# Optimization experiments

Measured on AMD Instinct MI355X. Metric: run time of the kernel, lower is better.

Reference implementation:

```python
import jax, jax.numpy as jnp
import numpy as np
import math

N_HEADS = 8

def setup_inputs() -> dict:
    key = jax.random.key(0)
    qkv = jax.random.normal(key, (4, 1536, 2048), dtype=jnp.float32)
    return {"qkv": qkv}

def reference(qkv) -> jnp.ndarray:
    bs, width, length = qkv.shape
    assert width % (3 * N_HEADS) == 0
    ch = width // (3 * N_HEADS)
    q, k, v = jnp.split(qkv, 3, axis=1)  # each [bs, n_heads*ch, length]
    scale = 1.0 / math.sqrt(math.sqrt(ch))
    q = (q * scale).reshape(bs * N_HEADS, ch, length)
    k = (k * scale).reshape(bs * N_HEADS, ch, length)
    v = v.reshape(bs * N_HEADS, ch, length)
    # scores: [B*H, t, s]
    weight = jnp.einsum('bct,bcs->bts', q, k)
    weight = jax.nn.softmax(weight, axis=-1)
    a = jnp.einsum('bts,bcs->bct', weight, v)  # [B*H, ch, length]
    return a.reshape(bs, -1, length)
```

## Files before the change

### kernel.cpp

```cpp
#include <hip/hip_runtime.h>
#include <hip/hip_bf16.h>

typedef unsigned short u16;
typedef unsigned int u32;
typedef __attribute__((ext_vector_type(8))) short short8;
typedef __attribute__((ext_vector_type(16))) float f32x16;

#define SEQ 2048

__device__ __forceinline__ u16 f2bf(float f) {
  union { __hip_bfloat16 h; u16 u; } c;
  c.h = __float2bfloat16(f);
  return c.u;
}

__device__ __forceinline__ float exp2fast(float x) {
  return __builtin_amdgcn_exp2f(x);
}

__global__ __launch_bounds__(256) void prep_qk(const float* __restrict__ qkv,
                                               u16* __restrict__ wsQ,
                                               u16* __restrict__ wsK) {
  __shared__ float tile[64 * 67];
  const int tid = threadIdx.x;
  const int t0 = blockIdx.x * 64;
  const int bh = blockIdx.y;
  const int b = bh >> 3, h = bh & 7;
  const int isK = blockIdx.z;
  const float scale = 0.42466090014692505f;
  const size_t inbase = ((size_t)b * 1536 + (size_t)isK * 512 + (size_t)h * 64) * SEQ;

  const int c = tid >> 2, tq = tid & 3;
#pragma unroll
  for (int u = 0; u < 4; ++u) {
    const int t = tq * 16 + u * 4;
    const float4 v = *(const float4*)(qkv + inbase + (size_t)c * SEQ + t0 + t);
    tile[c * 67 + t + 0] = v.x * scale;
    tile[c * 67 + t + 1] = v.y * scale;
    tile[c * 67 + t + 2] = v.z * scale;
    tile[c * 67 + t + 3] = v.w * scale;
  }
  __syncthreads();
  const int tt = tid >> 2, cq = tid & 3, c0 = cq * 16;
  u16* dst = (isK ? wsK : wsQ) + ((size_t)bh * SEQ + t0 + tt) * 64 + c0;
  union { u16 us[8]; uint4 v; } p0, p1;
#pragma unroll
  for (int i = 0; i < 8; ++i) p0.us[i] = f2bf(tile[(c0 + i) * 67 + tt]);
#pragma unroll
  for (int i = 0; i < 8; ++i) p1.us[i] = f2bf(tile[(c0 + 8 + i) * 67 + tt]);
  *(uint4*)(dst) = p0.v;
  *(uint4*)(dst + 8) = p1.v;
}

__global__ __launch_bounds__(256) void prep_v(const float* __restrict__ qkv,
                                              u16* __restrict__ wsV) {
  const int idx = blockIdx.x * 256 + threadIdx.x;
  const int s4 = idx & 511;
  const int cc = (idx >> 9) & 63;
  const int bh = idx >> 15;
  const int b = bh >> 3, h = bh & 7;
  const float4 v = *(const float4*)(qkv + (((size_t)b * 1536 + 1024 + (size_t)h * 64 + cc) * SEQ) + (size_t)s4 * 4);
  union { u16 us[4]; uint2 d; } pk;
  pk.us[0] = f2bf(v.x); pk.us[1] = f2bf(v.y); pk.us[2] = f2bf(v.z); pk.us[3] = f2bf(v.w);
  *(uint2*)(wsV + ((size_t)bh * 64 + cc) * SEQ + (size_t)s4 * 4) = pk.d;
}

__global__ __launch_bounds__(512, 2) void attn_kernel(const u16* __restrict__ wsQ,
                                                      const u16* __restrict__ wsK,
                                                      const u16* __restrict__ wsV,
                                                      float* __restrict__ out) {
  __shared__ __align__(16) char smem[65536];
  __shared__ float Xl[4][2][32];

  const int tid = threadIdx.x;
  const int w = tid >> 6;
  const int lane = tid & 63;
  const int tl = lane & 31;
  const int hi = lane >> 5;
  const int sh = w >> 2;
  const int u = w & 3;
  const int ts = tid & 255;

  const int bid = blockIdx.x;
  const int vb = (bid & 7) * 32 + (bid >> 3);
  const int tblk = vb & 7, bh = vb >> 3;
  const int tq0 = tblk * 256 + u * 64;

  const u16* qb = wsQ + (size_t)bh * (SEQ * 64);
  const u16* kb = wsK + (size_t)bh * (SEQ * 64);
  const u16* vbp = wsV + (size_t)bh * (SEQ * 64);

  char* KVs = smem + sh * 32768;

  short8 qf[2][4];
#pragma unroll
  for (int cb = 0; cb < 2; ++cb) {
    const u16* qrow = qb + (size_t)(tq0 + cb * 32 + tl) * 64 + 8 * hi;
#pragma unroll
    for (int ks = 0; ks < 4; ++ks) qf[cb][ks] = *(const short8*)(qrow + 16 * ks);
  }

  f32x16 acc[4];
#pragma unroll
  for (int a = 0; a < 4; ++a)
#pragma unroll
    for (int r = 0; r < 16; ++r) acc[a][r] = 0.0f;
  float la0[4] = {0, 0, 0, 0};
  float la1[4] = {0, 0, 0, 0};

  const int s_base = sh * 1024;
  const int srow = ts >> 3;
  uint4 kg[2], vg[2];

#define STAGE_LOAD(S)                                                       \
  do {                                                                      \
    _Pragma("unroll")                                                       \
    for (int _it = 0; _it < 2; ++_it) {                                     \
      const int _idx = _it * 256 + ts;                                      \
      const int _row = _idx >> 3, _g = _idx & 7;                            \
      kg[_it] = *(const uint4*)(kb + (size_t)((S) + _row) * 64 + _g * 8);   \
      vg[_it] = *(const uint4*)(vbp + (size_t)_row * SEQ + (S) + _g * 8);   \
    }                                                                       \
  } while (0)

#define STAGE_WRITE(PBUF)                                                   \
  do {                                                                      \
    char* _kd = KVs + (PBUF) * 16384;                                       \
    _Pragma("unroll")                                                       \
    for (int _it = 0; _it < 2; ++_it) {                                     \
      const int _idx = _it * 256 + ts;                                      \
      const int _row = _idx >> 3, _g = _idx & 7;                            \
      const int _sw = (_g ^ (_row & 7)) << 4;                               \
      *(uint4*)(_kd + _row * 128 + _sw) = kg[_it];                          \
      *(uint4*)(_kd + 8192 + _row * 128 + _sw) = vg[_it];                   \
    }                                                                       \
  } while (0)

#define PACK_P(PV16, PF0, PF1)                                                        \
  do {                                                                                \
    u32 _pk[8];                                                                       \
    _Pragma("unroll")                                                                 \
    for (int _q = 0; _q < 8; ++_q) {                                                  \
      const float _lo = PV16[2 * _q], _hi = PV16[2 * _q + 1];                         \
      asm("v_cvt_pk_bf16_f32 %0, %1, %2" : "=v"(_pk[_q]) : "v"(_lo), "v"(_hi));       \
    }                                                                                 \
    asm("v_permlane32_swap_b32 %0, %1" : "+v"(_pk[0]), "+v"(_pk[2]));                 \
    asm("v_permlane32_swap_b32 %0, %1" : "+v"(_pk[1]), "+v"(_pk[3]));                 \
    asm("v_permlane32_swap_b32 %0, %1" : "+v"(_pk[4]), "+v"(_pk[6]));                 \
    asm("v_permlane32_swap_b32 %0, %1" : "+v"(_pk[5]), "+v"(_pk[7]));                 \
    union { u32 u[4]; short8 v; } _f0, _f1;                                           \
    _f0.u[0] = _pk[0]; _f0.u[1] = _pk[1]; _f0.u[2] = _pk[2]; _f0.u[3] = _pk[3];       \
    _f1.u[0] = _pk[4]; _f1.u[1] = _pk[5]; _f1.u[2] = _pk[6]; _f1.u[3] = _pk[7];       \
    PF0 = _f0.v; PF1 = _f1.v;                                                         \
  } while (0)

  STAGE_LOAD(s_base);
  STAGE_WRITE(0);
  __syncthreads();

  int p = 0;
  for (int i = 0; i < 16; ++i) {
    if (i < 15) {
      const int snext = s_base + ((i + 1) << 6);
      STAGE_LOAD(snext);
    }

    const char* Ks = KVs + p * 16384;
    const char* Vs = Ks + 8192;

#pragma unroll
    for (int ss = 0; ss < 2; ++ss) {
      const int krow = ss * 32 + tl;
      short8 kf[4];
#pragma unroll
      for (int ks = 0; ks < 4; ++ks)
        kf[ks] = *(const short8*)(Ks + krow * 128 + (((2 * ks + hi) ^ (krow & 7)) << 4));

      f32x16 s0 = {0, 0, 0, 0, 0, 0, 0, 0, 0, 0, 0, 0, 0, 0, 0, 0};
      f32x16 s1 = s0;
      __builtin_amdgcn_s_setprio(1);
#pragma unroll
      for (int ks = 0; ks < 4; ++ks) {
        s0 = __builtin_amdgcn_mfma_f32_32x32x16_bf16(kf[ks], qf[0][ks], s0, 0, 0, 0);
        s1 = __builtin_amdgcn_mfma_f32_32x32x16_bf16(kf[ks], qf[1][ks], s1, 0, 0, 0);
      }
      __builtin_amdgcn_s_setprio(0);

#pragma unroll
      for (int r = 0; r < 16; ++r) s0[r] = exp2fast(s0[r]);
#pragma unroll
      for (int r = 0; r < 16; ++r) s1[r] = exp2fast(s1[r]);
#pragma unroll
      for (int j = 0; j < 4; ++j) {
        la0[j] += (s0[4 * j] + s0[4 * j + 1]) + (s0[4 * j + 2] + s0[4 * j + 3]);
        la1[j] += (s1[4 * j] + s1[4 * j + 1]) + (s1[4 * j + 2] + s1[4 * j + 3]);
      }

      short8 pf00, pf01, pf10, pf11;
      PACK_P(s0, pf00, pf01);
      PACK_P(s1, pf10, pf11);

      __builtin_amdgcn_s_setprio(1);
#pragma unroll
      for (int ct = 0; ct < 2; ++ct) {
        const int vrow = ct * 32 + tl;
#pragma unroll
        for (int ks2 = 0; ks2 < 2; ++ks2) {
          const int gr = ss * 4 + 2 * ks2 + hi;
          const short8 vf = *(const short8*)(Vs + vrow * 128 + ((gr ^ (vrow & 7)) << 4));
          acc[0 + ct] = __builtin_amdgcn_mfma_f32_32x32x16_bf16(vf, ks2 ? pf01 : pf00, acc[0 + ct], 0, 0, 0);
          acc[2 + ct] = __builtin_amdgcn_mfma_f32_32x32x16_bf16(vf, ks2 ? pf11 : pf10, acc[2 + ct], 0, 0, 0);
        }
      }
      __builtin_amdgcn_s_setprio(0);
    }

    if (i < 15) STAGE_WRITE(p ^ 1);
    __syncthreads();
    p ^= 1;
  }

  float l0 = (la0[0] + la0[1]) + (la0[2] + la0[3]);
  float l1 = (la1[0] + la1[1]) + (la1[2] + la1[3]);
  l0 += __shfl_xor(l0, 32, 64);
  l1 += __shfl_xor(l1, 32, 64);

  float* Xa = (float*)smem + u * 4096;
  if (sh == 1) {
#pragma unroll
    for (int a = 0; a < 4; ++a)
#pragma unroll
      for (int r = 0; r < 16; ++r) Xa[(a * 16 + r) * 64 + lane] = acc[a][r];
    Xl[u][0][tl] = l0;
    Xl[u][1][tl] = l1;
  }
  __syncthreads();
  if (sh == 0) {
    float* ob = out + (size_t)bh * 64 * SEQ;
    const float inv0 = 1.0f / (l0 + Xl[u][0][tl]);
    const float inv1 = 1.0f / (l1 + Xl[u][1][tl]);
#pragma unroll
    for (int ct = 0; ct < 2; ++ct)
#pragma unroll
      for (int r = 0; r < 16; ++r) {
        const int c = ct * 32 + (r & 3) + 8 * (r >> 2) + 4 * hi;
        const int ta = tq0 + tl, tb2 = tq0 + 32 + tl;
        ob[(size_t)c * SEQ + ta] = (acc[0 + ct][r] + Xa[((0 + ct) * 16 + r) * 64 + lane]) * inv0;
        ob[(size_t)c * SEQ + tb2] = (acc[2 + ct][r] + Xa[((2 + ct) * 16 + r) * 64 + lane]) * inv1;
      }
  }
}

extern "C" void kernel_launch(void* const* d_in, const int* in_sizes, int n_in,
                              void* d_out, int out_size, void* d_ws, size_t ws_size,
                              hipStream_t stream) {
  const float* qkv = (const float*)d_in[0];
  float* out = (float*)d_out;
  u16* wsQ = (u16*)d_ws;
  u16* wsK = wsQ + (size_t)32 * SEQ * 64;
  u16* wsV = wsK + (size_t)32 * SEQ * 64;

  prep_qk<<<dim3(32, 32, 2), 256, 0, stream>>>(qkv, wsQ, wsK);
  prep_v<<<4096, 256, 0, stream>>>(qkv, wsV);
  attn_kernel<<<256, 512, 0, stream>>>(wsQ, wsK, wsV, out);
}
```

Baseline: 60.65 us.

## Pre-swizzle K/V into LDS-ready chunks and stage with global_load_lds

The prep kernels now write K and V into a combined workspace laid out in 32KB chunks that already match the swizzled shared-memory layout. The attention kernel copies each chunk straight into LDS with global_load_lds, removing the register round-trip of the old load-then-write staging. The grid grows to 512 blocks of 128 queries each, with four waves splitting the keys per unit and a two-step cross-wave reduction at the end. The launch bounds ask for four blocks per CU, which may raise occupancy but adds register pressure, more reduction work, and more blocks re-reading K/V.

```diff
diff --git a/kernel.cpp b/kernel.cpp
--- a/kernel.cpp
+++ b/kernel.cpp
@@ -18,9 +18,10 @@
   return __builtin_amdgcn_exp2f(x);
 }
 
+
 __global__ __launch_bounds__(256) void prep_qk(const float* __restrict__ qkv,
                                                u16* __restrict__ wsQ,
-                                               u16* __restrict__ wsK) {
+                                               u16* __restrict__ wsKV) {
   __shared__ float tile[64 * 67];
   const int tid = threadIdx.x;
   const int t0 = blockIdx.x * 64;
@@ -41,56 +42,74 @@
     tile[c * 67 + t + 3] = v.w * scale;
   }
   __syncthreads();
-  const int tt = tid >> 2, cq = tid & 3, c0 = cq * 16;
-  u16* dst = (isK ? wsK : wsQ) + ((size_t)bh * SEQ + t0 + tt) * 64 + c0;
-  union { u16 us[8]; uint4 v; } p0, p1;
-#pragma unroll
-  for (int i = 0; i < 8; ++i) p0.us[i] = f2bf(tile[(c0 + i) * 67 + tt]);
-#pragma unroll
-  for (int i = 0; i < 8; ++i) p1.us[i] = f2bf(tile[(c0 + 8 + i) * 67 + tt]);
-  *(uint4*)(dst) = p0.v;
-  *(uint4*)(dst + 8) = p1.v;
+
+  if (isK) {
+    const int tt = tid >> 2, cq = tid & 3;
+    const int j = (t0 >> 5) + (tt >> 5);
+    const int row = tt & 31;
+    u16* base = wsKV + (size_t)bh * 262144
+              + (size_t)(j >> 2) * 16384 + (size_t)((j >> 1) & 1) * 8192
+              + (size_t)(j & 1) * 2048 + row * 64;
+    union { u16 us[8]; uint4 q; } g0, g1;
+#pragma unroll
+    for (int e = 0; e < 8; ++e) g0.us[e] = f2bf(tile[(cq * 16 + e) * 67 + tt]);
+#pragma unroll
+    for (int e = 0; e < 8; ++e) g1.us[e] = f2bf(tile[(cq * 16 + 8 + e) * 67 + tt]);
+    *(uint4*)(base + (((2 * cq) ^ (row & 7)) << 3)) = g0.q;
+    *(uint4*)(base + (((2 * cq + 1) ^ (row & 7)) << 3)) = g1.q;
+  } else {
+    const int tt = tid >> 2, cq = tid & 3, c0 = cq * 16;
+    u16* dst = wsQ + ((size_t)bh * SEQ + t0 + tt) * 64 + c0;
+    union { u16 us[8]; uint4 v; } p0, p1;
+#pragma unroll
+    for (int i = 0; i < 8; ++i) p0.us[i] = f2bf(tile[(c0 + i) * 67 + tt]);
+#pragma unroll
+    for (int i = 0; i < 8; ++i) p1.us[i] = f2bf(tile[(c0 + 8 + i) * 67 + tt]);
+    *(uint4*)(dst) = p0.v;
+    *(uint4*)(dst + 8) = p1.v;
+  }
 }
 
 __global__ __launch_bounds__(256) void prep_v(const float* __restrict__ qkv,
-                                              u16* __restrict__ wsV) {
+                                              u16* __restrict__ wsKV) {
   const int idx = blockIdx.x * 256 + threadIdx.x;
-  const int s4 = idx & 511;
-  const int cc = (idx >> 9) & 63;
-  const int bh = idx >> 15;
+  const int sg = idx & 7;
+  const int g64 = (idx >> 3) & 31;
+  const int cc = (idx >> 8) & 63;
+  const int bh = idx >> 14;
   const int b = bh >> 3, h = bh & 7;
-  const float4 v = *(const float4*)(qkv + (((size_t)b * 1536 + 1024 + (size_t)h * 64 + cc) * SEQ) + (size_t)s4 * 4);
-  union { u16 us[4]; uint2 d; } pk;
-  pk.us[0] = f2bf(v.x); pk.us[1] = f2bf(v.y); pk.us[2] = f2bf(v.z); pk.us[3] = f2bf(v.w);
-  *(uint2*)(wsV + ((size_t)bh * 64 + cc) * SEQ + (size_t)s4 * 4) = pk.d;
-}
-
-__global__ __launch_bounds__(512, 2) void attn_kernel(const u16* __restrict__ wsQ,
-                                                      const u16* __restrict__ wsK,
-                                                      const u16* __restrict__ wsV,
+  const float* src = qkv + ((size_t)b * 1536 + 1024 + (size_t)h * 64 + cc) * SEQ + g64 * 64 + sg * 8;
+  const float4 v0 = *(const float4*)(src);
+  const float4 v1 = *(const float4*)(src + 4);
+  union { u16 us[8]; uint4 q; } pk;
+  pk.us[0] = f2bf(v0.x); pk.us[1] = f2bf(v0.y); pk.us[2] = f2bf(v0.z); pk.us[3] = f2bf(v0.w);
+  pk.us[4] = f2bf(v1.x); pk.us[5] = f2bf(v1.y); pk.us[6] = f2bf(v1.z); pk.us[7] = f2bf(v1.w);
+  u16* dst = wsKV + (size_t)bh * 262144 + (size_t)(g64 >> 1) * 16384 + (size_t)(g64 & 1) * 8192
+           + 4096 + cc * 64 + ((sg ^ (cc & 7)) << 3);
+  *(uint4*)dst = pk.q;
+}
+
+__global__ __launch_bounds__(512, 4) void attn_kernel(const u16* __restrict__ wsQ,
+                                                      const u16* __restrict__ wsKV,
                                                       float* __restrict__ out) {
   __shared__ __align__(16) char smem[65536];
-  __shared__ float Xl[4][2][32];
+  __shared__ float Xl[2][2][2][32];
 
   const int tid = threadIdx.x;
   const int w = tid >> 6;
   const int lane = tid & 63;
   const int tl = lane & 31;
   const int hi = lane >> 5;
-  const int sh = w >> 2;
-  const int u = w & 3;
-  const int ts = tid & 255;
+  const int unit = w >> 2;
+  const int sp = w & 3;
 
   const int bid = blockIdx.x;
-  const int vb = (bid & 7) * 32 + (bid >> 3);
-  const int tblk = vb & 7, bh = vb >> 3;
-  const int tq0 = tblk * 256 + u * 64;
+  const int vb = (bid & 7) * 64 + (bid >> 3);
+  const int tbp = vb & 15, bh = vb >> 4;
+  const int tq0 = tbp * 128 + unit * 64;
 
   const u16* qb = wsQ + (size_t)bh * (SEQ * 64);
-  const u16* kb = wsK + (size_t)bh * (SEQ * 64);
-  const u16* vbp = wsV + (size_t)bh * (SEQ * 64);
-
-  char* KVs = smem + sh * 32768;
+  const char* kvb = (const char*)(wsKV + (size_t)bh * 262144);
 
   short8 qf[2][4];
 #pragma unroll
@@ -108,32 +127,15 @@
   float la0[4] = {0, 0, 0, 0};
   float la1[4] = {0, 0, 0, 0};
 
-  const int s_base = sh * 1024;
-  const int srow = ts >> 3;
-  uint4 kg[2], vg[2];
-
-#define STAGE_LOAD(S)                                                       \
-  do {                                                                      \
-    _Pragma("unroll")                                                       \
-    for (int _it = 0; _it < 2; ++_it) {                                     \
-      const int _idx = _it * 256 + ts;                                      \
-      const int _row = _idx >> 3, _g = _idx & 7;                            \
-      kg[_it] = *(const uint4*)(kb + (size_t)((S) + _row) * 64 + _g * 8);   \
-      vg[_it] = *(const uint4*)(vbp + (size_t)_row * SEQ + (S) + _g * 8);   \
-    }                                                                       \
-  } while (0)
-
-#define STAGE_WRITE(PBUF)                                                   \
-  do {                                                                      \
-    char* _kd = KVs + (PBUF) * 16384;                                       \
-    _Pragma("unroll")                                                       \
-    for (int _it = 0; _it < 2; ++_it) {                                     \
-      const int _idx = _it * 256 + ts;                                      \
-      const int _row = _idx >> 3, _g = _idx & 7;                            \
-      const int _sw = (_g ^ (_row & 7)) << 4;                               \
-      *(uint4*)(_kd + _row * 128 + _sw) = kg[_it];                          \
-      *(uint4*)(_kd + 8192 + _row * 128 + _sw) = vg[_it];                   \
-    }                                                                       \
+#define STAGE(QUAD, BUF)                                                              \
+  do {                                                                                \
+    const char* _s = kvb + (size_t)(QUAD) * 32768 + w * 4096 + lane * 16;             \
+    char* _d = smem + (BUF) * 32768 + w * 4096;                                       \
+    _Pragma("unroll")                                                                 \
+    for (int _c = 0; _c < 4; ++_c)                                                    \
+      __builtin_amdgcn_global_load_lds(                                               \
+          (__attribute__((address_space(1))) void*)(_s + _c * 1024),                  \
+          (__attribute__((address_space(3))) void*)(_d + _c * 1024), 16, 0, 0);       \
   } while (0)
 
 #define PACK_P(PV16, PF0, PF1)                                                        \
@@ -154,70 +156,60 @@
     PF0 = _f0.v; PF1 = _f1.v;                                                         \
   } while (0)
 
-  STAGE_LOAD(s_base);
-  STAGE_WRITE(0);
-  __syncthreads();
-
-  int p = 0;
+  STAGE(0, 0);
+  __syncthreads();
+
   for (int i = 0; i < 16; ++i) {
-    if (i < 15) {
-      const int snext = s_base + ((i + 1) << 6);
-      STAGE_LOAD(snext);
-    }
-
-    const char* Ks = KVs + p * 16384;
-    const char* Vs = Ks + 8192;
-
-#pragma unroll
-    for (int ss = 0; ss < 2; ++ss) {
-      const int krow = ss * 32 + tl;
-      short8 kf[4];
-#pragma unroll
-      for (int ks = 0; ks < 4; ++ks)
-        kf[ks] = *(const short8*)(Ks + krow * 128 + (((2 * ks + hi) ^ (krow & 7)) << 4));
-
-      f32x16 s0 = {0, 0, 0, 0, 0, 0, 0, 0, 0, 0, 0, 0, 0, 0, 0, 0};
-      f32x16 s1 = s0;
-      __builtin_amdgcn_s_setprio(1);
-#pragma unroll
-      for (int ks = 0; ks < 4; ++ks) {
-        s0 = __builtin_amdgcn_mfma_f32_32x32x16_bf16(kf[ks], qf[0][ks], s0, 0, 0, 0);
-        s1 = __builtin_amdgcn_mfma_f32_32x32x16_bf16(kf[ks], qf[1][ks], s1, 0, 0, 0);
+    if (i < 15) STAGE(i + 1, (i + 1) & 1);
+
+    const char* grp = smem + (i & 1) * 32768 + (sp >> 1) * 16384;
+    const char* Ks = grp + (sp & 1) * 4096;
+    const char* Vs = grp + 8192;
+
+    short8 kf[4];
+#pragma unroll
+    for (int ks = 0; ks < 4; ++ks)
+      kf[ks] = *(const short8*)(Ks + tl * 128 + (((2 * ks + hi) ^ (tl & 7)) << 4));
+
+    f32x16 s0 = {0, 0, 0, 0, 0, 0, 0, 0, 0, 0, 0, 0, 0, 0, 0, 0};
+    f32x16 s1 = s0;
+    __builtin_amdgcn_s_setprio(1);
+#pragma unroll
+    for (int ks = 0; ks < 4; ++ks) {
+      s0 = __builtin_amdgcn_mfma_f32_32x32x16_bf16(kf[ks], qf[0][ks], s0, 0, 0, 0);
+      s1 = __builtin_amdgcn_mfma_f32_32x32x16_bf16(kf[ks], qf[1][ks], s1, 0, 0, 0);
+    }
+    __builtin_amdgcn_s_setprio(0);
+
+#pragma unroll
+    for (int r = 0; r < 16; ++r) s0[r] = exp2fast(s0[r]);
+#pragma unroll
+    for (int r = 0; r < 16; ++r) s1[r] = exp2fast(s1[r]);
+#pragma unroll
+    for (int j = 0; j < 4; ++j) {
+      la0[j] += (s0[4 * j] + s0[4 * j + 1]) + (s0[4 * j + 2] + s0[4 * j + 3]);
+      la1[j] += (s1[4 * j] + s1[4 * j + 1]) + (s1[4 * j + 2] + s1[4 * j + 3]);
+    }
+
+    short8 pf00, pf01, pf10, pf11;
+    PACK_P(s0, pf00, pf01);
+    PACK_P(s1, pf10, pf11);
+
+    __builtin_amdgcn_s_setprio(1);
+#pragma unroll
+    for (int ct = 0; ct < 2; ++ct) {
+      const int vrow = ct * 32 + tl;
+#pragma unroll
+      for (int ks2 = 0; ks2 < 2; ++ks2) {
+        const int gr = (sp & 1) * 4 + 2 * ks2 + hi;
+        const short8 vf = *(const short8*)(Vs + vrow * 128 + ((gr ^ (vrow & 7)) << 4));
+        acc[0 + ct] = __builtin_amdgcn_mfma_f32_32x32x16_bf16(vf, ks2 ? pf01 : pf00, acc[0 + ct], 0, 0, 0);
+        acc[2 + ct] = __builtin_amdgcn_mfma_f32_32x32x16_bf16(vf, ks2 ? pf11 : pf10, acc[2 + ct], 0, 0, 0);
       }
-      __builtin_amdgcn_s_setprio(0);
-
-#pragma unroll
-      for (int r = 0; r < 16; ++r) s0[r] = exp2fast(s0[r]);
-#pragma unroll
-      for (int r = 0; r < 16; ++r) s1[r] = exp2fast(s1[r]);
-#pragma unroll
-      for (int j = 0; j < 4; ++j) {
-        la0[j] += (s0[4 * j] + s0[4 * j + 1]) + (s0[4 * j + 2] + s0[4 * j + 3]);
-        la1[j] += (s1[4 * j] + s1[4 * j + 1]) + (s1[4 * j + 2] + s1[4 * j + 3]);
-      }
-
-      short8 pf00, pf01, pf10, pf11;
-      PACK_P(s0, pf00, pf01);
-      PACK_P(s1, pf10, pf11);
-
-      __builtin_amdgcn_s_setprio(1);
-#pragma unroll
-      for (int ct = 0; ct < 2; ++ct) {
-        const int vrow = ct * 32 + tl;
-#pragma unroll
-        for (int ks2 = 0; ks2 < 2; ++ks2) {
-          const int gr = ss * 4 + 2 * ks2 + hi;
-          const short8 vf = *(const short8*)(Vs + vrow * 128 + ((gr ^ (vrow & 7)) << 4));
-          acc[0 + ct] = __builtin_amdgcn_mfma_f32_32x32x16_bf16(vf, ks2 ? pf01 : pf00, acc[0 + ct], 0, 0, 0);
-          acc[2 + ct] = __builtin_amdgcn_mfma_f32_32x32x16_bf16(vf, ks2 ? pf11 : pf10, acc[2 + ct], 0, 0, 0);
-        }
-      }
-      __builtin_amdgcn_s_setprio(0);
-    }
-
-    if (i < 15) STAGE_WRITE(p ^ 1);
+    }
+    __builtin_amdgcn_s_setprio(0);
+
     __syncthreads();
-    p ^= 1;
   }
 
   float l0 = (la0[0] + la0[1]) + (la0[2] + la0[3]);
@@ -225,29 +217,48 @@
   l0 += __shfl_xor(l0, 32, 64);
   l1 += __shfl_xor(l1, 32, 64);
 
-  float* Xa = (float*)smem + u * 4096;
-  if (sh == 1) {
+  if (sp >= 2) {
+    float* Xa = (float*)smem + (size_t)(unit * 2 + (sp - 2)) * 4096;
 #pragma unroll
     for (int a = 0; a < 4; ++a)
 #pragma unroll
       for (int r = 0; r < 16; ++r) Xa[(a * 16 + r) * 64 + lane] = acc[a][r];
-    Xl[u][0][tl] = l0;
-    Xl[u][1][tl] = l1;
-  }
-  __syncthreads();
-  if (sh == 0) {
+    Xl[unit][sp - 2][0][tl] = l0;
+    Xl[unit][sp - 2][1][tl] = l1;
+  }
+  __syncthreads();
+  if (sp < 2) {
+    float* Xa = (float*)smem + (size_t)(unit * 2 + sp) * 4096;
+#pragma unroll
+    for (int a = 0; a < 4; ++a)
+#pragma unroll
+      for (int r = 0; r < 16; ++r) acc[a][r] += Xa[(a * 16 + r) * 64 + lane];
+    l0 += Xl[unit][sp][0][tl];
+    l1 += Xl[unit][sp][1][tl];
+    if (sp == 1) {
+#pragma unroll
+      for (int a = 0; a < 4; ++a)
+#pragma unroll
+        for (int r = 0; r < 16; ++r) Xa[(a * 16 + r) * 64 + lane] = acc[a][r];
+      Xl[unit][1][0][tl] = l0;
+      Xl[unit][1][1][tl] = l1;
+    }
+  }
+  __syncthreads();
+  if (sp == 0) {
+    const float* Xa = (const float*)smem + (size_t)(unit * 2 + 1) * 4096;
     float* ob = out + (size_t)bh * 64 * SEQ;
-    const float inv0 = 1.0f / (l0 + Xl[u][0][tl]);
-    const float inv1 = 1.0f / (l1 + Xl[u][1][tl]);
-#pragma unroll
-    for (int ct = 0; ct < 2; ++ct)
-#pragma unroll
-      for (int r = 0; r < 16; ++r) {
-        const int c = ct * 32 + (r & 3) + 8 * (r >> 2) + 4 * hi;
-        const int ta = tq0 + tl, tb2 = tq0 + 32 + tl;
-        ob[(size_t)c * SEQ + ta] = (acc[0 + ct][r] + Xa[((0 + ct) * 16 + r) * 64 + lane]) * inv0;
-        ob[(size_t)c * SEQ + tb2] = (acc[2 + ct][r] + Xa[((2 + ct) * 16 + r) * 64 + lane]) * inv1;
-      }
+    const float inv0 = 1.0f / (l0 + Xl[unit][1][0][tl]);
+    const float inv1 = 1.0f / (l1 + Xl[unit][1][1][tl]);
+#pragma unroll
+    for (int r = 0; r < 16; ++r) {
+      const int c0 = (r & 3) + 8 * (r >> 2) + 4 * hi;
+      const int ta = tq0 + tl, tb2 = tq0 + 32 + tl;
+      ob[(size_t)c0 * SEQ + ta] = (acc[0][r] + Xa[(0 * 16 + r) * 64 + lane]) * inv0;
+      ob[(size_t)(c0 + 32) * SEQ + ta] = (acc[1][r] + Xa[(1 * 16 + r) * 64 + lane]) * inv0;
+      ob[(size_t)c0 * SEQ + tb2] = (acc[2][r] + Xa[(2 * 16 + r) * 64 + lane]) * inv1;
+      ob[(size_t)(c0 + 32) * SEQ + tb2] = (acc[3][r] + Xa[(3 * 16 + r) * 64 + lane]) * inv1;
+    }
   }
 }
 
@@ -257,10 +268,9 @@
   const float* qkv = (const float*)d_in[0];
   float* out = (float*)d_out;
   u16* wsQ = (u16*)d_ws;
-  u16* wsK = wsQ + (size_t)32 * SEQ * 64;
-  u16* wsV = wsK + (size_t)32 * SEQ * 64;
-
-  prep_qk<<<dim3(32, 32, 2), 256, 0, stream>>>(qkv, wsQ, wsK);
-  prep_v<<<4096, 256, 0, stream>>>(qkv, wsV);
-  attn_kernel<<<256, 512, 0, stream>>>(wsQ, wsK, wsV, out);
-}
+  u16* wsKV = wsQ + (size_t)32 * SEQ * 64;
+
+  prep_qk<<<dim3(32, 32, 2), 256, 0, stream>>>(qkv, wsQ, wsKV);
+  prep_v<<<2048, 256, 0, stream>>>(qkv, wsKV);
+  attn_kernel<<<512, 512, 0, stream>>>(wsQ, wsKV, out);
+}
```

Result: slower. 124.9 us (+105.9%).

## Pre-swizzle V into MFMA fragment order and load it directly from global

Applied to the files above, without the earlier changes.

prep_v now writes V in a layout that matches the per-lane MFMA operand order, so each lane reads its fragments with one contiguous 16-byte global load. V no longer goes through LDS, which halves LDS use per block and removes the V LDS writes and reads. The launch bound drops its min-blocks hint. In exchange, V loads issue from global/L2 inside the inner loop with less latency hiding, and the prep kernel loses its fully coalesced reads.

```diff
diff --git a/kernel.cpp b/kernel.cpp
--- a/kernel.cpp
+++ b/kernel.cpp
@@ -55,20 +55,29 @@
 __global__ __launch_bounds__(256) void prep_v(const float* __restrict__ qkv,
                                               u16* __restrict__ wsV) {
   const int idx = blockIdx.x * 256 + threadIdx.x;
-  const int s4 = idx & 511;
-  const int cc = (idx >> 9) & 63;
-  const int bh = idx >> 15;
+  const int slot = idx & 255;
+  const int sb32 = (idx >> 8) & 63;
+  const int bh = idx >> 14;
+  const int lane = slot & 63;
+  const int ctks = slot >> 6;
+  const int ct = ctks >> 1, ks2 = ctks & 1;
+  const int hi = lane >> 5, tl = lane & 31;
+  const int cc = ct * 32 + tl;
+  const int s = sb32 * 32 + ks2 * 16 + hi * 8;
   const int b = bh >> 3, h = bh & 7;
-  const float4 v = *(const float4*)(qkv + (((size_t)b * 1536 + 1024 + (size_t)h * 64 + cc) * SEQ) + (size_t)s4 * 4);
-  union { u16 us[4]; uint2 d; } pk;
-  pk.us[0] = f2bf(v.x); pk.us[1] = f2bf(v.y); pk.us[2] = f2bf(v.z); pk.us[3] = f2bf(v.w);
-  *(uint2*)(wsV + ((size_t)bh * 64 + cc) * SEQ + (size_t)s4 * 4) = pk.d;
-}
-
-__global__ __launch_bounds__(512, 2) void attn_kernel(const u16* __restrict__ wsQ,
-                                                      const u16* __restrict__ wsK,
-                                                      const u16* __restrict__ wsV,
-                                                      float* __restrict__ out) {
+  const float* src = qkv + ((size_t)b * 1536 + 1024 + (size_t)h * 64 + cc) * SEQ + s;
+  const float4 v0 = *(const float4*)(src);
+  const float4 v1 = *(const float4*)(src + 4);
+  union { u16 us[8]; uint4 q; } pk;
+  pk.us[0] = f2bf(v0.x); pk.us[1] = f2bf(v0.y); pk.us[2] = f2bf(v0.z); pk.us[3] = f2bf(v0.w);
+  pk.us[4] = f2bf(v1.x); pk.us[5] = f2bf(v1.y); pk.us[6] = f2bf(v1.z); pk.us[7] = f2bf(v1.w);
+  *(uint4*)(wsV + (size_t)idx * 8) = pk.q;
+}
+
+__global__ __launch_bounds__(512) void attn_kernel(const u16* __restrict__ wsQ,
+                                                   const u16* __restrict__ wsK,
+                                                   const u16* __restrict__ wsV,
+                                                   float* __restrict__ out) {
   __shared__ __align__(16) char smem[65536];
   __shared__ float Xl[4][2][32];
 
@@ -88,9 +97,9 @@
 
   const u16* qb = wsQ + (size_t)bh * (SEQ * 64);
   const u16* kb = wsK + (size_t)bh * (SEQ * 64);
-  const u16* vbp = wsV + (size_t)bh * (SEQ * 64);
-
-  char* KVs = smem + sh * 32768;
+  const u16* vstream = wsV + (size_t)bh * 131072 + lane * 8;
+
+  char* Kbuf = smem + sh * 16384;
 
   short8 qf[2][4];
 #pragma unroll
@@ -108,9 +117,7 @@
   float la0[4] = {0, 0, 0, 0};
   float la1[4] = {0, 0, 0, 0};
 
-  const int s_base = sh * 1024;
-  const int srow = ts >> 3;
-  uint4 kg[2], vg[2];
+  uint4 kg[2];
 
 #define STAGE_LOAD(S)                                                       \
   do {                                                                      \
@@ -119,20 +126,17 @@
       const int _idx = _it * 256 + ts;                                      \
       const int _row = _idx >> 3, _g = _idx & 7;                            \
       kg[_it] = *(const uint4*)(kb + (size_t)((S) + _row) * 64 + _g * 8);   \
-      vg[_it] = *(const uint4*)(vbp + (size_t)_row * SEQ + (S) + _g * 8);   \
     }                                                                       \
   } while (0)
 
 #define STAGE_WRITE(PBUF)                                                   \
   do {                                                                      \
-    char* _kd = KVs + (PBUF) * 16384;                                       \
+    char* _kd = Kbuf + (PBUF) * 8192;                                       \
     _Pragma("unroll")                                                       \
     for (int _it = 0; _it < 2; ++_it) {                                     \
       const int _idx = _it * 256 + ts;                                      \
       const int _row = _idx >> 3, _g = _idx & 7;                            \
-      const int _sw = (_g ^ (_row & 7)) << 4;                               \
-      *(uint4*)(_kd + _row * 128 + _sw) = kg[_it];                          \
-      *(uint4*)(_kd + 8192 + _row * 128 + _sw) = vg[_it];                   \
+      *(uint4*)(_kd + _row * 128 + ((_g ^ (_row & 7)) << 4)) = kg[_it];     \
     }                                                                       \
   } while (0)
 
@@ -154,19 +158,15 @@
     PF0 = _f0.v; PF1 = _f1.v;                                                         \
   } while (0)
 
-  STAGE_LOAD(s_base);
+  STAGE_LOAD(sh * 1024);
   STAGE_WRITE(0);
   __syncthreads();
 
-  int p = 0;
   for (int i = 0; i < 16; ++i) {
-    if (i < 15) {
-      const int snext = s_base + ((i + 1) << 6);
-      STAGE_LOAD(snext);
-    }
-
-    const char* Ks = KVs + p * 16384;
-    const char* Vs = Ks + 8192;
+    if (i < 15) STAGE_LOAD(sh * 1024 + (i + 1) * 64);
+
+    const char* Ks = Kbuf + (i & 1) * 8192;
+    const int jbase = sh * 32 + i * 2;
 
 #pragma unroll
     for (int ss = 0; ss < 2; ++ss) {
@@ -186,6 +186,12 @@
       }
       __builtin_amdgcn_s_setprio(0);
 
+      const u16* vp = vstream + (size_t)(jbase + ss) * 2048;
+      const short8 vf0 = *(const short8*)(vp);
+      const short8 vf1 = *(const short8*)(vp + 512);
+      const short8 vf2 = *(const short8*)(vp + 1024);
+      const short8 vf3 = *(const short8*)(vp + 1536);
+
 #pragma unroll
       for (int r = 0; r < 16; ++r) s0[r] = exp2fast(s0[r]);
 #pragma unroll
@@ -201,23 +207,19 @@
       PACK_P(s1, pf10, pf11);
 
       __builtin_amdgcn_s_setprio(1);
-#pragma unroll
-      for (int ct = 0; ct < 2; ++ct) {
-        const int vrow = ct * 32 + tl;
-#pragma unroll
-        for (int ks2 = 0; ks2 < 2; ++ks2) {
-          const int gr = ss * 4 + 2 * ks2 + hi;
-          const short8 vf = *(const short8*)(Vs + vrow * 128 + ((gr ^ (vrow & 7)) << 4));
-          acc[0 + ct] = __builtin_amdgcn_mfma_f32_32x32x16_bf16(vf, ks2 ? pf01 : pf00, acc[0 + ct], 0, 0, 0);
-          acc[2 + ct] = __builtin_amdgcn_mfma_f32_32x32x16_bf16(vf, ks2 ? pf11 : pf10, acc[2 + ct], 0, 0, 0);
-        }
-      }
+      acc[0] = __builtin_amdgcn_mfma_f32_32x32x16_bf16(vf0, pf00, acc[0], 0, 0, 0);
+      acc[0] = __builtin_amdgcn_mfma_f32_32x32x16_bf16(vf1, pf01, acc[0], 0, 0, 0);
+      acc[1] = __builtin_amdgcn_mfma_f32_32x32x16_bf16(vf2, pf00, acc[1], 0, 0, 0);
+      acc[1] = __builtin_amdgcn_mfma_f32_32x32x16_bf16(vf3, pf01, acc[1], 0, 0, 0);
+      acc[2] = __builtin_amdgcn_mfma_f32_32x32x16_bf16(vf0, pf10, acc[2], 0, 0, 0);
+      acc[2] = __builtin_amdgcn_mfma_f32_32x32x16_bf16(vf1, pf11, acc[2], 0, 0, 0);
+      acc[3] = __builtin_amdgcn_mfma_f32_32x32x16_bf16(vf2, pf10, acc[3], 0, 0, 0);
+      acc[3] = __builtin_amdgcn_mfma_f32_32x32x16_bf16(vf3, pf11, acc[3], 0, 0, 0);
       __builtin_amdgcn_s_setprio(0);
     }
 
-    if (i < 15) STAGE_WRITE(p ^ 1);
+    if (i < 15) STAGE_WRITE((i + 1) & 1);
     __syncthreads();
-    p ^= 1;
   }
 
   float l0 = (la0[0] + la0[1]) + (la0[2] + la0[3]);
@@ -240,14 +242,14 @@
     const float inv0 = 1.0f / (l0 + Xl[u][0][tl]);
     const float inv1 = 1.0f / (l1 + Xl[u][1][tl]);
 #pragma unroll
-    for (int ct = 0; ct < 2; ++ct)
-#pragma unroll
-      for (int r = 0; r < 16; ++r) {
-        const int c = ct * 32 + (r & 3) + 8 * (r >> 2) + 4 * hi;
-        const int ta = tq0 + tl, tb2 = tq0 + 32 + tl;
-        ob[(size_t)c * SEQ + ta] = (acc[0 + ct][r] + Xa[((0 + ct) * 16 + r) * 64 + lane]) * inv0;
-        ob[(size_t)c * SEQ + tb2] = (acc[2 + ct][r] + Xa[((2 + ct) * 16 + r) * 64 + lane]) * inv1;
-      }
+    for (int r = 0; r < 16; ++r) {
+      const int c0 = (r & 3) + 8 * (r >> 2) + 4 * hi;
+      const int ta = tq0 + tl, tb2 = tq0 + 32 + tl;
+      ob[(size_t)c0 * SEQ + ta] = (acc[0][r] + Xa[(0 * 16 + r) * 64 + lane]) * inv0;
+      ob[(size_t)(c0 + 32) * SEQ + ta] = (acc[1][r] + Xa[(1 * 16 + r) * 64 + lane]) * inv0;
+      ob[(size_t)c0 * SEQ + tb2] = (acc[2][r] + Xa[(2 * 16 + r) * 64 + lane]) * inv1;
+      ob[(size_t)(c0 + 32) * SEQ + tb2] = (acc[3][r] + Xa[(3 * 16 + r) * 64 + lane]) * inv1;
+    }
   }
 }
 
@@ -261,6 +263,6 @@
   u16* wsV = wsK + (size_t)32 * SEQ * 64;
 
   prep_qk<<<dim3(32, 32, 2), 256, 0, stream>>>(qkv, wsQ, wsK);
-  prep_v<<<4096, 256, 0, stream>>>(qkv, wsV);
+  prep_v<<<2048, 256, 0, stream>>>(qkv, wsV);
   attn_kernel<<<256, 512, 0, stream>>>(wsQ, wsK, wsV, out);
 }
```

Result: faster. 58.91 us (-2.9%).
